# Kernel tuning notes

Hardware: AMD Instinct MI355X
Metric: run time of the kernel (lower is better)

The kernel has to match this reference:

```python
import jax, jax.numpy as jnp
import numpy as np

N_NODES = 100000
N_EDGES = 1600000
D = 128


def setup_inputs() -> dict:
    key = jax.random.key(0)
    ks = jax.random.split(key, 8)
    s = lambda fan_in: 1.0 / np.sqrt(fan_in)
    return {
        "node_feature": jax.random.normal(ks[0], (N_NODES, D), dtype=jnp.float32),
        "src": jax.random.randint(ks[1], (N_EDGES,), 0, N_NODES),
        "dst": jax.random.randint(ks[2], (N_EDGES,), 0, N_NODES),
        "W1": jax.random.normal(ks[3], (2 * D, D), dtype=jnp.float32) * s(2 * D),
        "b1": jnp.zeros((D,), dtype=jnp.float32),
        "W2": jax.random.normal(ks[4], (D, D), dtype=jnp.float32) * s(D),
        "b2": jnp.zeros((D,), dtype=jnp.float32),
        "W3": jax.random.normal(ks[5], (D, D), dtype=jnp.float32) * s(D),
        "b3": jnp.zeros((D,), dtype=jnp.float32),
    }


def reference(node_feature, src, dst, W1, b1, W2, b2, W3, b3):
    n_nodes = node_feature.shape[0]
    # message: gather src node features over edges  [E, D]
    msg = node_feature[src]
    # reduce: sum messages into destination nodes   [N, D]
    agg = jax.ops.segment_sum(msg, dst, num_segments=n_nodes)
    # apply: concat(aggregated, own) -> MLP         [N, 2D] -> [N, D]
    inp = jnp.concatenate([agg, node_feature], axis=-1)
    h = jax.nn.relu(inp @ W1 + b1)
    h = jax.nn.relu(h @ W2 + b2)
    return h @ W3 + b3
```

## Files before the change

kernel.cpp:

```cpp
#include <hip/hip_runtime.h>

#define NNODES 100000
#define NEDGES 1600000
#define DD 128
#define BM 64
#define NBUCK 98
#define NBLK_MLP ((NNODES + BM - 1) / BM)
#define CAP 32
#define CAPB 20480
#define BIN1_WGS 200
#define BIN1_EPW 8192

#define WS_GCUR 100000
#define WS_BBASE 100128
#define WS_OFFS 100352
#define WS_ESRC 201216

#define WT1HI 0
#define WT1LO 32768
#define WT2HI 65536
#define WT2LO 81920
#define WT3HI 98304
#define WT3LO 114688

typedef __attribute__((ext_vector_type(8))) short short8;
typedef __attribute__((ext_vector_type(4))) float f32x4;

__device__ __forceinline__ void bf16_split(float x, ushort& hi, ushort& lo) {
  unsigned u = __float_as_uint(x);
  ushort h = (ushort)((u + 0x7FFFu + ((u >> 16) & 1u)) >> 16);
  float r = x - __uint_as_float(((unsigned)h) << 16);
  unsigned v = __float_as_uint(r);
  ushort l = (ushort)((v + 0x7FFFu + ((v >> 16) & 1u)) >> 16);
  hi = h;
  lo = l;
}

__device__ __forceinline__ void split8(const float4 v0, const float4 v1,
                                       short8& hi, short8& lo) {
  float x[8] = {v0.x, v0.y, v0.z, v0.w, v1.x, v1.y, v1.z, v1.w};
#pragma unroll
  for (int j = 0; j < 8; ++j) {
    ushort h, l;
    bf16_split(x[j], h, l);
    hi[j] = (short)h;
    lo[j] = (short)l;
  }
}

__global__ __launch_bounds__(256) void bin1_kernel(const int* __restrict__ src,
                                                   const int* __restrict__ dst,
                                                   int* __restrict__ gcur,
                                                   unsigned* __restrict__ ebuf) {
  __shared__ unsigned stage[NBUCK][CAP];
  __shared__ int scnt[NBUCK];
  const int t = threadIdx.x;
  for (int i = t; i < NBUCK; i += 256) scnt[i] = 0;
  __syncthreads();
  const int e0 = blockIdx.x * BIN1_EPW;
  for (int r = 0; r < BIN1_EPW / 1024; ++r) {
    unsigned item[4];
    int buck[4];
    int pend[4];
#pragma unroll
    for (int j = 0; j < 4; ++j) {
      pend[j] = 0;
      int e = e0 + r * 1024 + j * 256 + t;
      if (e < NEDGES) {
        int d = dst[e];
        int s = src[e];
        buck[j] = d >> 10;
        item[j] = ((unsigned)(d & 1023) << 17) | (unsigned)s;
        int p = atomicAdd(&scnt[buck[j]], 1);
        if (p < CAP)
          stage[buck[j]][p] = item[j];
        else
          pend[j] = 1;
      }
    }
    int pendLeft;
    do {
      __syncthreads();
      if (t < NBUCK && scnt[t] >= CAP) {
        int base = t * CAPB + atomicAdd(&gcur[t], CAP);
        for (int q = 0; q < CAP; ++q) ebuf[base + q] = stage[t][q];
        scnt[t] = 0;
      }
      __syncthreads();
      int mypend = 0;
#pragma unroll
      for (int j = 0; j < 4; ++j) {
        if (pend[j]) {
          int p = atomicAdd(&scnt[buck[j]], 1);
          if (p < CAP) {
            stage[buck[j]][p] = item[j];
            pend[j] = 0;
          } else {
            mypend = 1;
          }
        }
      }
      pendLeft = __syncthreads_count(mypend);
    } while (pendLeft > 0);
  }
  __syncthreads();
  if (t < NBUCK) {
    int n = scnt[t];
    if (n > 0) {
      int base = t * CAPB + atomicAdd(&gcur[t], n);
      for (int q = 0; q < n; ++q) ebuf[base + q] = stage[t][q];
    }
  }
}

__global__ __launch_bounds__(128) void bscan_kernel(const int* __restrict__ gcur,
                                                    int* __restrict__ bbase,
                                                    int* __restrict__ offs) {
  __shared__ int s[128];
  const int t = threadIdx.x;
  int v = (t < NBUCK) ? gcur[t] : 0;
  s[t] = v;
  __syncthreads();
  for (int off = 1; off < 128; off <<= 1) {
    int u = (t >= off) ? s[t - off] : 0;
    __syncthreads();
    s[t] += u;
    __syncthreads();
  }
  if (t < NBUCK) bbase[t] = s[t] - v;
  if (t == NBUCK - 1) offs[NNODES] = s[t];
}

__global__ __launch_bounds__(1024) void bucket_csr_kernel(const unsigned* __restrict__ ebuf,
                                                          const int* __restrict__ gcur,
                                                          const int* __restrict__ bbase,
                                                          int* __restrict__ offs,
                                                          int* __restrict__ esrc) {
  __shared__ int h[1024];
  __shared__ int cur[1024];
  const int t = threadIdx.x;
  const int c = blockIdx.x;
  const int n = gcur[c];
  const unsigned* eb = ebuf + c * CAPB;
  h[t] = 0;
  __syncthreads();
  for (int i = t; i < n; i += 1024) atomicAdd(&h[eb[i] >> 17], 1);
  __syncthreads();
  int v = h[t];
  for (int off = 1; off < 1024; off <<= 1) {
    int u = (t >= off) ? h[t - off] : 0;
    __syncthreads();
    h[t] += u;
    __syncthreads();
  }
  int excl = h[t] - v + bbase[c];
  int node = (c << 10) + t;
  if (node < NNODES) offs[node] = excl;
  cur[t] = excl;
  __syncthreads();
  for (int i = t; i < n; i += 1024) {
    unsigned e = eb[i];
    int p = atomicAdd(&cur[e >> 17], 1);
    esrc[p] = (int)(e & 0x1FFFFu);
  }
}

__global__ __launch_bounds__(256) void agg_kernel(const float* __restrict__ nf,
                                                  const int* __restrict__ offs,
                                                  const int* __restrict__ esrc,
                                                  float* __restrict__ agg) {
  const int t = threadIdx.x;
  const int node = blockIdx.x * 8 + (t >> 5);
  const int c4 = (t & 31) << 2;
  const int beg = offs[node];
  const int end = offs[node + 1];
  float4 a0 = make_float4(0.f, 0.f, 0.f, 0.f);
  float4 a1 = make_float4(0.f, 0.f, 0.f, 0.f);
  float4 a2 = make_float4(0.f, 0.f, 0.f, 0.f);
  float4 a3 = make_float4(0.f, 0.f, 0.f, 0.f);
  int i = beg;
  for (; i + 3 < end; i += 4) {
    int s0 = esrc[i];
    int s1 = esrc[i + 1];
    int s2 = esrc[i + 2];
    int s3 = esrc[i + 3];
    float4 v0 = *(const float4*)&nf[s0 * DD + c4];
    float4 v1 = *(const float4*)&nf[s1 * DD + c4];
    float4 v2 = *(const float4*)&nf[s2 * DD + c4];
    float4 v3 = *(const float4*)&nf[s3 * DD + c4];
    a0.x += v0.x; a0.y += v0.y; a0.z += v0.z; a0.w += v0.w;
    a1.x += v1.x; a1.y += v1.y; a1.z += v1.z; a1.w += v1.w;
    a2.x += v2.x; a2.y += v2.y; a2.z += v2.z; a2.w += v2.w;
    a3.x += v3.x; a3.y += v3.y; a3.z += v3.z; a3.w += v3.w;
  }
  for (; i < end; ++i) {
    int s0 = esrc[i];
    float4 v0 = *(const float4*)&nf[s0 * DD + c4];
    a0.x += v0.x; a0.y += v0.y; a0.z += v0.z; a0.w += v0.w;
  }
  a0.x += a1.x; a0.y += a1.y; a0.z += a1.z; a0.w += a1.w;
  a2.x += a3.x; a2.y += a3.y; a2.z += a3.z; a2.w += a3.w;
  a0.x += a2.x; a0.y += a2.y; a0.z += a2.z; a0.w += a2.w;
  *(float4*)&agg[node * DD + c4] = a0;
}

__global__ __launch_bounds__(256) void wprep_kernel(const float* __restrict__ W1,
                                                    const float* __restrict__ W2,
                                                    const float* __restrict__ W3,
                                                    ushort* __restrict__ wt) {
  int tid = blockIdx.x * 256 + threadIdx.x;
  const float* W;
  int dstHi, dstLo, k, col;
  if (tid < 32768) {
    int j = tid & 7, l = (tid >> 3) & 63, tile = tid >> 9;
    int kk = tile & 7, c16 = tile >> 3;
    k = kk * 32 + (l >> 4) * 8 + j;
    col = c16 * 16 + (l & 15);
    W = W1;
    dstHi = WT1HI + tid;
    dstLo = WT1LO + tid;
  } else {
    int t2 = tid - 32768;
    int which = t2 >> 14;
    int t1 = t2 & 16383;
    int j = t1 & 7, l = (t1 >> 3) & 63, tile = t1 >> 9;
    int kk = tile & 3, c16 = tile >> 2;
    k = kk * 32 + (l >> 4) * 8 + j;
    col = c16 * 16 + (l & 15);
    W = which ? W3 : W2;
    dstHi = (which ? WT3HI : WT2HI) + t1;
    dstLo = (which ? WT3LO : WT2LO) + t1;
  }
  ushort hi, lo;
  bf16_split(W[k * DD + col], hi, lo);
  wt[dstHi] = hi;
  wt[dstLo] = lo;
}

__device__ __forceinline__ void store_h(ushort* Hh, ushort* Hl,
                                        const float* __restrict__ b,
                                        int wr, int wc, int l15, int lhi,
                                        f32x4 acc[2][4]) {
#pragma unroll
  for (int rt = 0; rt < 2; ++rt) {
#pragma unroll
    for (int ct = 0; ct < 4; ++ct) {
      int col = wc * 64 + ct * 16 + l15;
      float bias = b[col];
#pragma unroll
      for (int i = 0; i < 4; ++i) {
        int row = wr * 32 + rt * 16 + lhi * 4 + i;
        float v = fmaxf(acc[rt][ct][i] + bias, 0.f);
        ushort h, l;
        bf16_split(v, h, l);
        int byte = (row * 256 + col * 2) ^ ((row & 7) << 4);
        *(ushort*)((char*)Hh + byte) = h;
        *(ushort*)((char*)Hl + byte) = l;
      }
    }
  }
}

__device__ __forceinline__ void l1_step(const float* __restrict__ srcb,
                                        const ushort* __restrict__ wt,
                                        int kkTile, int kOff, const int rowA[2],
                                        int wc, int lane, int lhi,
                                        f32x4 acc[2][4]) {
  short8 ahi[2], alo[2];
#pragma unroll
  for (int rt = 0; rt < 2; ++rt) {
    const float* p = srcb + rowA[rt] * DD + kOff + lhi * 8;
    float4 v0 = *(const float4*)p;
    float4 v1 = *(const float4*)(p + 4);
    split8(v0, v1, ahi[rt], alo[rt]);
  }
#pragma unroll
  for (int ct = 0; ct < 4; ++ct) {
    int tb = ((wc * 4 + ct) * 8 + kkTile) * 512 + lane * 8;
    short8 bhi = *(const short8*)&wt[WT1HI + tb];
    short8 blo = *(const short8*)&wt[WT1LO + tb];
#pragma unroll
    for (int rt = 0; rt < 2; ++rt) {
      acc[rt][ct] = __builtin_amdgcn_mfma_f32_16x16x32_bf16(ahi[rt], bhi, acc[rt][ct], 0, 0, 0);
      acc[rt][ct] = __builtin_amdgcn_mfma_f32_16x16x32_bf16(ahi[rt], blo, acc[rt][ct], 0, 0, 0);
      acc[rt][ct] = __builtin_amdgcn_mfma_f32_16x16x32_bf16(alo[rt], bhi, acc[rt][ct], 0, 0, 0);
    }
  }
}

__device__ __forceinline__ void layer_lds(const ushort* Hh, const ushort* Hl,
                                          const ushort* __restrict__ WhiT,
                                          const ushort* __restrict__ WloT,
                                          int wr, int wc, int lane, int l15,
                                          int lhi, f32x4 acc[2][4]) {
#pragma unroll 2
  for (int kk = 0; kk < 4; ++kk) {
    short8 ahi[2], alo[2];
#pragma unroll
    for (int rt = 0; rt < 2; ++rt) {
      int row = wr * 32 + rt * 16 + l15;
      int byte = (row * 256 + kk * 64 + lhi * 16) ^ ((row & 7) << 4);
      ahi[rt] = *(const short8*)((const char*)Hh + byte);
      alo[rt] = *(const short8*)((const char*)Hl + byte);
    }
#pragma unroll
    for (int ct = 0; ct < 4; ++ct) {
      int tb = ((wc * 4 + ct) * 4 + kk) * 512 + lane * 8;
      short8 bhi = *(const short8*)&WhiT[tb];
      short8 blo = *(const short8*)&WloT[tb];
#pragma unroll
      for (int rt = 0; rt < 2; ++rt) {
        acc[rt][ct] = __builtin_amdgcn_mfma_f32_16x16x32_bf16(ahi[rt], bhi, acc[rt][ct], 0, 0, 0);
        acc[rt][ct] = __builtin_amdgcn_mfma_f32_16x16x32_bf16(ahi[rt], blo, acc[rt][ct], 0, 0, 0);
        acc[rt][ct] = __builtin_amdgcn_mfma_f32_16x16x32_bf16(alo[rt], bhi, acc[rt][ct], 0, 0, 0);
      }
    }
  }
}

__global__ __launch_bounds__(256, 4) void mlp_kernel(const float* __restrict__ agg,
                                                     const float* __restrict__ nf,
                                                     const ushort* __restrict__ wt,
                                                     const float* __restrict__ b1,
                                                     const float* __restrict__ b2,
                                                     const float* __restrict__ b3,
                                                     float* __restrict__ out) {
  __shared__ ushort smem[16384];
  ushort* Hhi = smem;
  ushort* Hlo = smem + 8192;

  const int t = threadIdx.x;
  const int lane = t & 63;
  const int w = t >> 6;
  const int wr = w & 1;
  const int wc = w >> 1;
  const int l15 = lane & 15;
  const int lhi = lane >> 4;
  const int base = blockIdx.x * BM;

  int rowA[2];
  {
    int r0 = base + wr * 32 + l15;
    rowA[0] = min(r0, NNODES - 1);
    rowA[1] = min(r0 + 16, NNODES - 1);
  }

  const f32x4 z = {0.f, 0.f, 0.f, 0.f};
  f32x4 acc[2][4];

#pragma unroll
  for (int rt = 0; rt < 2; ++rt)
#pragma unroll
    for (int ct = 0; ct < 4; ++ct) acc[rt][ct] = z;
#pragma unroll 2
  for (int kk = 0; kk < 4; ++kk)
    l1_step(agg, wt, kk, kk * 32, rowA, wc, lane, lhi, acc);
#pragma unroll 2
  for (int kk = 0; kk < 4; ++kk)
    l1_step(nf, wt, kk + 4, kk * 32, rowA, wc, lane, lhi, acc);
  store_h(Hhi, Hlo, b1, wr, wc, l15, lhi, acc);
  __syncthreads();

#pragma unroll
  for (int rt = 0; rt < 2; ++rt)
#pragma unroll
    for (int ct = 0; ct < 4; ++ct) acc[rt][ct] = z;
  layer_lds(Hhi, Hlo, wt + WT2HI, wt + WT2LO, wr, wc, lane, l15, lhi, acc);
  __syncthreads();
  store_h(Hhi, Hlo, b2, wr, wc, l15, lhi, acc);
  __syncthreads();

#pragma unroll
  for (int rt = 0; rt < 2; ++rt)
#pragma unroll
    for (int ct = 0; ct < 4; ++ct) acc[rt][ct] = z;
  layer_lds(Hhi, Hlo, wt + WT3HI, wt + WT3LO, wr, wc, lane, l15, lhi, acc);
#pragma unroll
  for (int rt = 0; rt < 2; ++rt) {
#pragma unroll
    for (int ct = 0; ct < 4; ++ct) {
      int col = wc * 64 + ct * 16 + l15;
      float bias = b3[col];
#pragma unroll
      for (int i = 0; i < 4; ++i) {
        int row = base + wr * 32 + rt * 16 + lhi * 4 + i;
        if (row < NNODES) out[row * DD + col] = acc[rt][ct][i] + bias;
      }
    }
  }
}

extern "C" void kernel_launch(void* const* d_in, const int* in_sizes, int n_in,
                              void* d_out, int out_size, void* d_ws, size_t ws_size,
                              hipStream_t stream) {
  const float* nf = (const float*)d_in[0];
  const int* src = (const int*)d_in[1];
  const int* dst = (const int*)d_in[2];
  const float* W1 = (const float*)d_in[3];
  const float* b1 = (const float*)d_in[4];
  const float* W2 = (const float*)d_in[5];
  const float* b2 = (const float*)d_in[6];
  const float* W3 = (const float*)d_in[7];
  const float* b3 = (const float*)d_in[8];
  float* out = (float*)d_out;

  int* wsi = (int*)d_ws;
  int* gcur = wsi + WS_GCUR;
  int* bbase = wsi + WS_BBASE;
  int* offs = wsi + WS_OFFS;
  int* esrc = wsi + WS_ESRC;
  ushort* wt = (ushort*)wsi;

  unsigned* ebuf = (unsigned*)out;
  float* agg = out;

  hipMemsetAsync(gcur, 0, NBUCK * sizeof(int), stream);
  bin1_kernel<<<BIN1_WGS, 256, 0, stream>>>(src, dst, gcur, ebuf);
  bscan_kernel<<<1, 128, 0, stream>>>(gcur, bbase, offs);
  bucket_csr_kernel<<<NBUCK, 1024, 0, stream>>>(ebuf, gcur, bbase, offs, esrc);
  wprep_kernel<<<256, 256, 0, stream>>>(W1, W2, W3, wt);
  agg_kernel<<<NNODES / 8, 256, 0, stream>>>(nf, offs, esrc, agg);
  mlp_kernel<<<NBLK_MLP, 256, 0, stream>>>(agg, nf, wt, b1, b2, b3, out);
}
```

Measured before the change: 253.9 us.

## Fuse neighbor aggregation into MLP kernel via LDS-staged bf16 split tiles

Removes the separate aggregation kernel. Each MLP block now gathers and sums the neighbor features for its 64 nodes directly into shared memory as hi/lo bf16 pairs. Layer 1 reads that aggregated half from LDS instead of from a global agg buffer, which avoids writing and re-reading a 51MB intermediate. In exchange, each block runs a long irregular gather phase before its MFMA work, with fewer warps in flight per node (8 nodes per 32-lane group run serially), which may lower memory-level parallelism for the gather.

```diff
diff --git a/kernel.cpp b/kernel.cpp
--- a/kernel.cpp
+++ b/kernel.cpp
@@ -163,45 +163,6 @@
     int p = atomicAdd(&cur[e >> 17], 1);
     esrc[p] = (int)(e & 0x1FFFFu);
   }
-}
-
-__global__ __launch_bounds__(256) void agg_kernel(const float* __restrict__ nf,
-                                                  const int* __restrict__ offs,
-                                                  const int* __restrict__ esrc,
-                                                  float* __restrict__ agg) {
-  const int t = threadIdx.x;
-  const int node = blockIdx.x * 8 + (t >> 5);
-  const int c4 = (t & 31) << 2;
-  const int beg = offs[node];
-  const int end = offs[node + 1];
-  float4 a0 = make_float4(0.f, 0.f, 0.f, 0.f);
-  float4 a1 = make_float4(0.f, 0.f, 0.f, 0.f);
-  float4 a2 = make_float4(0.f, 0.f, 0.f, 0.f);
-  float4 a3 = make_float4(0.f, 0.f, 0.f, 0.f);
-  int i = beg;
-  for (; i + 3 < end; i += 4) {
-    int s0 = esrc[i];
-    int s1 = esrc[i + 1];
-    int s2 = esrc[i + 2];
-    int s3 = esrc[i + 3];
-    float4 v0 = *(const float4*)&nf[s0 * DD + c4];
-    float4 v1 = *(const float4*)&nf[s1 * DD + c4];
-    float4 v2 = *(const float4*)&nf[s2 * DD + c4];
-    float4 v3 = *(const float4*)&nf[s3 * DD + c4];
-    a0.x += v0.x; a0.y += v0.y; a0.z += v0.z; a0.w += v0.w;
-    a1.x += v1.x; a1.y += v1.y; a1.z += v1.z; a1.w += v1.w;
-    a2.x += v2.x; a2.y += v2.y; a2.z += v2.z; a2.w += v2.w;
-    a3.x += v3.x; a3.y += v3.y; a3.z += v3.z; a3.w += v3.w;
-  }
-  for (; i < end; ++i) {
-    int s0 = esrc[i];
-    float4 v0 = *(const float4*)&nf[s0 * DD + c4];
-    a0.x += v0.x; a0.y += v0.y; a0.z += v0.z; a0.w += v0.w;
-  }
-  a0.x += a1.x; a0.y += a1.y; a0.z += a1.z; a0.w += a1.w;
-  a2.x += a3.x; a2.y += a3.y; a2.z += a3.z; a2.w += a3.w;
-  a0.x += a2.x; a0.y += a2.y; a0.z += a2.z; a0.w += a2.w;
-  *(float4*)&agg[node * DD + c4] = a0;
 }
 
 __global__ __launch_bounds__(256) void wprep_kernel(const float* __restrict__ W1,
@@ -237,6 +198,65 @@
   wt[dstLo] = lo;
 }
 
+
+template <int KT>
+__device__ __forceinline__ void lds_ksteps(const ushort* Hh, const ushort* Hl,
+                                           const ushort* __restrict__ WhiT,
+                                           const ushort* __restrict__ WloT,
+                                           int tileOff, int wr, int wc, int lane,
+                                           int l15, int lhi, f32x4 acc[2][4]) {
+#pragma unroll 2
+  for (int kk = 0; kk < 4; ++kk) {
+    short8 ahi[2], alo[2];
+#pragma unroll
+    for (int rt = 0; rt < 2; ++rt) {
+      int row = wr * 32 + rt * 16 + l15;
+      int byte = (row * 256 + kk * 64 + lhi * 16) ^ ((row & 7) << 4);
+      ahi[rt] = *(const short8*)((const char*)Hh + byte);
+      alo[rt] = *(const short8*)((const char*)Hl + byte);
+    }
+#pragma unroll
+    for (int ct = 0; ct < 4; ++ct) {
+      int tb = ((wc * 4 + ct) * KT + tileOff + kk) * 512 + lane * 8;
+      short8 bhi = *(const short8*)&WhiT[tb];
+      short8 blo = *(const short8*)&WloT[tb];
+#pragma unroll
+      for (int rt = 0; rt < 2; ++rt) {
+        acc[rt][ct] = __builtin_amdgcn_mfma_f32_16x16x32_bf16(ahi[rt], bhi, acc[rt][ct], 0, 0, 0);
+        acc[rt][ct] = __builtin_amdgcn_mfma_f32_16x16x32_bf16(ahi[rt], blo, acc[rt][ct], 0, 0, 0);
+        acc[rt][ct] = __builtin_amdgcn_mfma_f32_16x16x32_bf16(alo[rt], bhi, acc[rt][ct], 0, 0, 0);
+      }
+    }
+  }
+}
+
+__device__ __forceinline__ void l1_step(const float* __restrict__ srcb,
+                                        const ushort* __restrict__ wt,
+                                        int kkTile, int kOff, const int rowA[2],
+                                        int wc, int lane, int lhi,
+                                        f32x4 acc[2][4]) {
+  short8 ahi[2], alo[2];
+#pragma unroll
+  for (int rt = 0; rt < 2; ++rt) {
+    const float* p = srcb + rowA[rt] * DD + kOff + lhi * 8;
+    float4 v0 = *(const float4*)p;
+    float4 v1 = *(const float4*)(p + 4);
+    split8(v0, v1, ahi[rt], alo[rt]);
+  }
+#pragma unroll
+  for (int ct = 0; ct < 4; ++ct) {
+    int tb = ((wc * 4 + ct) * 8 + kkTile) * 512 + lane * 8;
+    short8 bhi = *(const short8*)&wt[WT1HI + tb];
+    short8 blo = *(const short8*)&wt[WT1LO + tb];
+#pragma unroll
+    for (int rt = 0; rt < 2; ++rt) {
+      acc[rt][ct] = __builtin_amdgcn_mfma_f32_16x16x32_bf16(ahi[rt], bhi, acc[rt][ct], 0, 0, 0);
+      acc[rt][ct] = __builtin_amdgcn_mfma_f32_16x16x32_bf16(ahi[rt], blo, acc[rt][ct], 0, 0, 0);
+      acc[rt][ct] = __builtin_amdgcn_mfma_f32_16x16x32_bf16(alo[rt], bhi, acc[rt][ct], 0, 0, 0);
+    }
+  }
+}
+
 __device__ __forceinline__ void store_h(ushort* Hh, ushort* Hl,
                                         const float* __restrict__ b,
                                         int wr, int wc, int l15, int lhi,
@@ -261,73 +281,17 @@
   }
 }
 
-__device__ __forceinline__ void l1_step(const float* __restrict__ srcb,
-                                        const ushort* __restrict__ wt,
-                                        int kkTile, int kOff, const int rowA[2],
-                                        int wc, int lane, int lhi,
-                                        f32x4 acc[2][4]) {
-  short8 ahi[2], alo[2];
-#pragma unroll
-  for (int rt = 0; rt < 2; ++rt) {
-    const float* p = srcb + rowA[rt] * DD + kOff + lhi * 8;
-    float4 v0 = *(const float4*)p;
-    float4 v1 = *(const float4*)(p + 4);
-    split8(v0, v1, ahi[rt], alo[rt]);
-  }
-#pragma unroll
-  for (int ct = 0; ct < 4; ++ct) {
-    int tb = ((wc * 4 + ct) * 8 + kkTile) * 512 + lane * 8;
-    short8 bhi = *(const short8*)&wt[WT1HI + tb];
-    short8 blo = *(const short8*)&wt[WT1LO + tb];
-#pragma unroll
-    for (int rt = 0; rt < 2; ++rt) {
-      acc[rt][ct] = __builtin_amdgcn_mfma_f32_16x16x32_bf16(ahi[rt], bhi, acc[rt][ct], 0, 0, 0);
-      acc[rt][ct] = __builtin_amdgcn_mfma_f32_16x16x32_bf16(ahi[rt], blo, acc[rt][ct], 0, 0, 0);
-      acc[rt][ct] = __builtin_amdgcn_mfma_f32_16x16x32_bf16(alo[rt], bhi, acc[rt][ct], 0, 0, 0);
-    }
-  }
-}
-
-__device__ __forceinline__ void layer_lds(const ushort* Hh, const ushort* Hl,
-                                          const ushort* __restrict__ WhiT,
-                                          const ushort* __restrict__ WloT,
-                                          int wr, int wc, int lane, int l15,
-                                          int lhi, f32x4 acc[2][4]) {
-#pragma unroll 2
-  for (int kk = 0; kk < 4; ++kk) {
-    short8 ahi[2], alo[2];
-#pragma unroll
-    for (int rt = 0; rt < 2; ++rt) {
-      int row = wr * 32 + rt * 16 + l15;
-      int byte = (row * 256 + kk * 64 + lhi * 16) ^ ((row & 7) << 4);
-      ahi[rt] = *(const short8*)((const char*)Hh + byte);
-      alo[rt] = *(const short8*)((const char*)Hl + byte);
-    }
-#pragma unroll
-    for (int ct = 0; ct < 4; ++ct) {
-      int tb = ((wc * 4 + ct) * 4 + kk) * 512 + lane * 8;
-      short8 bhi = *(const short8*)&WhiT[tb];
-      short8 blo = *(const short8*)&WloT[tb];
-#pragma unroll
-      for (int rt = 0; rt < 2; ++rt) {
-        acc[rt][ct] = __builtin_amdgcn_mfma_f32_16x16x32_bf16(ahi[rt], bhi, acc[rt][ct], 0, 0, 0);
-        acc[rt][ct] = __builtin_amdgcn_mfma_f32_16x16x32_bf16(ahi[rt], blo, acc[rt][ct], 0, 0, 0);
-        acc[rt][ct] = __builtin_amdgcn_mfma_f32_16x16x32_bf16(alo[rt], bhi, acc[rt][ct], 0, 0, 0);
-      }
-    }
-  }
-}
-
-__global__ __launch_bounds__(256, 4) void mlp_kernel(const float* __restrict__ agg,
-                                                     const float* __restrict__ nf,
-                                                     const ushort* __restrict__ wt,
-                                                     const float* __restrict__ b1,
-                                                     const float* __restrict__ b2,
-                                                     const float* __restrict__ b3,
-                                                     float* __restrict__ out) {
+__global__ __launch_bounds__(256, 4) void fused_kernel(const float* __restrict__ nf,
+                                                       const int* __restrict__ offs,
+                                                       const int* __restrict__ esrc,
+                                                       const ushort* __restrict__ wt,
+                                                       const float* __restrict__ b1,
+                                                       const float* __restrict__ b2,
+                                                       const float* __restrict__ b3,
+                                                       float* __restrict__ out) {
   __shared__ ushort smem[16384];
-  ushort* Hhi = smem;
-  ushort* Hlo = smem + 8192;
+  ushort* Xhi = smem;
+  ushort* Xlo = smem + 8192;
 
   const int t = threadIdx.x;
   const int lane = t & 63;
@@ -338,6 +302,56 @@
   const int lhi = lane >> 4;
   const int base = blockIdx.x * BM;
 
+  {
+    const int g = t >> 5;
+    const int l32 = t & 31;
+    const int col = l32 << 2;
+    for (int j = 0; j < 8; ++j) {
+      const int r = g * 8 + j;
+      const int node = base + r;
+      float4 a0 = make_float4(0.f, 0.f, 0.f, 0.f);
+      float4 a1 = make_float4(0.f, 0.f, 0.f, 0.f);
+      float4 a2 = make_float4(0.f, 0.f, 0.f, 0.f);
+      float4 a3 = make_float4(0.f, 0.f, 0.f, 0.f);
+      if (node < NNODES) {
+        const int beg = offs[node];
+        const int end = offs[node + 1];
+        int i = beg;
+        for (; i + 3 < end; i += 4) {
+          int s0 = esrc[i];
+          int s1 = esrc[i + 1];
+          int s2 = esrc[i + 2];
+          int s3 = esrc[i + 3];
+          float4 v0 = *(const float4*)&nf[s0 * DD + col];
+          float4 v1 = *(const float4*)&nf[s1 * DD + col];
+          float4 v2 = *(const float4*)&nf[s2 * DD + col];
+          float4 v3 = *(const float4*)&nf[s3 * DD + col];
+          a0.x += v0.x; a0.y += v0.y; a0.z += v0.z; a0.w += v0.w;
+          a1.x += v1.x; a1.y += v1.y; a1.z += v1.z; a1.w += v1.w;
+          a2.x += v2.x; a2.y += v2.y; a2.z += v2.z; a2.w += v2.w;
+          a3.x += v3.x; a3.y += v3.y; a3.z += v3.z; a3.w += v3.w;
+        }
+        for (; i < end; ++i) {
+          int s0 = esrc[i];
+          float4 v0 = *(const float4*)&nf[s0 * DD + col];
+          a0.x += v0.x; a0.y += v0.y; a0.z += v0.z; a0.w += v0.w;
+        }
+      }
+      a0.x += a1.x; a0.y += a1.y; a0.z += a1.z; a0.w += a1.w;
+      a2.x += a3.x; a2.y += a3.y; a2.z += a3.z; a2.w += a3.w;
+      a0.x += a2.x; a0.y += a2.y; a0.z += a2.z; a0.w += a2.w;
+      ushort h0, h1, h2, h3, l0, l1, l2, l3;
+      bf16_split(a0.x, h0, l0);
+      bf16_split(a0.y, h1, l1);
+      bf16_split(a0.z, h2, l2);
+      bf16_split(a0.w, h3, l3);
+      int byte = (r * 256 + col * 2) ^ ((r & 7) << 4);
+      *(ushort4*)((char*)Xhi + byte) = make_ushort4(h0, h1, h2, h3);
+      *(ushort4*)((char*)Xlo + byte) = make_ushort4(l0, l1, l2, l3);
+    }
+  }
+  __syncthreads();
+
   int rowA[2];
   {
     int r0 = base + wr * 32 + l15;
@@ -352,29 +366,28 @@
   for (int rt = 0; rt < 2; ++rt)
 #pragma unroll
     for (int ct = 0; ct < 4; ++ct) acc[rt][ct] = z;
-#pragma unroll 2
-  for (int kk = 0; kk < 4; ++kk)
-    l1_step(agg, wt, kk, kk * 32, rowA, wc, lane, lhi, acc);
+  lds_ksteps<8>(Xhi, Xlo, wt + WT1HI, wt + WT1LO, 0, wr, wc, lane, l15, lhi, acc);
 #pragma unroll 2
   for (int kk = 0; kk < 4; ++kk)
     l1_step(nf, wt, kk + 4, kk * 32, rowA, wc, lane, lhi, acc);
-  store_h(Hhi, Hlo, b1, wr, wc, l15, lhi, acc);
+  __syncthreads();
+  store_h(Xhi, Xlo, b1, wr, wc, l15, lhi, acc);
   __syncthreads();
 
 #pragma unroll
   for (int rt = 0; rt < 2; ++rt)
 #pragma unroll
     for (int ct = 0; ct < 4; ++ct) acc[rt][ct] = z;
-  layer_lds(Hhi, Hlo, wt + WT2HI, wt + WT2LO, wr, wc, lane, l15, lhi, acc);
-  __syncthreads();
-  store_h(Hhi, Hlo, b2, wr, wc, l15, lhi, acc);
+  lds_ksteps<4>(Xhi, Xlo, wt + WT2HI, wt + WT2LO, 0, wr, wc, lane, l15, lhi, acc);
+  __syncthreads();
+  store_h(Xhi, Xlo, b2, wr, wc, l15, lhi, acc);
   __syncthreads();
 
 #pragma unroll
   for (int rt = 0; rt < 2; ++rt)
 #pragma unroll
     for (int ct = 0; ct < 4; ++ct) acc[rt][ct] = z;
-  layer_lds(Hhi, Hlo, wt + WT3HI, wt + WT3LO, wr, wc, lane, l15, lhi, acc);
+  lds_ksteps<4>(Xhi, Xlo, wt + WT3HI, wt + WT3LO, 0, wr, wc, lane, l15, lhi, acc);
 #pragma unroll
   for (int rt = 0; rt < 2; ++rt) {
 #pragma unroll
@@ -412,13 +425,11 @@
   ushort* wt = (ushort*)wsi;
 
   unsigned* ebuf = (unsigned*)out;
-  float* agg = out;
 
   hipMemsetAsync(gcur, 0, NBUCK * sizeof(int), stream);
   bin1_kernel<<<BIN1_WGS, 256, 0, stream>>>(src, dst, gcur, ebuf);
   bscan_kernel<<<1, 128, 0, stream>>>(gcur, bbase, offs);
   bucket_csr_kernel<<<NBUCK, 1024, 0, stream>>>(ebuf, gcur, bbase, offs, esrc);
   wprep_kernel<<<256, 256, 0, stream>>>(W1, W2, W3, wt);
-  agg_kernel<<<NNODES / 8, 256, 0, stream>>>(nf, offs, esrc, agg);
-  mlp_kernel<<<NBLK_MLP, 256, 0, stream>>>(agg, nf, wt, b1, b2, b3, out);
-}
+  fused_kernel<<<NBLK_MLP, 256, 0, stream>>>(nf, offs, esrc, wt, b1, b2, b3, out);
+}
```

Result: faster. 240.3 us (-5.4%).
